# Kernel tuning notes

Hardware: AMD Instinct MI355X
Metric: run time of the kernel (lower is better)

Reference implementation:

```python
import jax, jax.numpy as jnp
import numpy as np

TEMPERATURE = 8.0  # sqrt(d_k), d_k = 64
MINIMUM_VALUE = -1e9  # stand-in for C.MINIMUM_VALUE


def setup_inputs() -> dict:
    key = jax.random.key(0)
    kq, kk, kv, km = jax.random.split(key, 4)
    B, N, D = 32, 2048, 64
    q = jax.random.normal(kq, (B, N, D), dtype=jnp.float32)
    k = jax.random.normal(kk, (B, N, D), dtype=jnp.float32)
    v = jax.random.normal(kv, (B, N, D), dtype=jnp.float32)
    mask = jax.random.randint(km, (B, N, N), 0, 2, dtype=jnp.int32)
    return {"q": q, "k": k, "v": v, "mask": mask}


def reference(q, k, v, mask):
    # scores: [B, Nq, Nk]
    attn = jnp.einsum("bqd,bkd->bqk", q, k) / TEMPERATURE
    attn = jnp.where(mask > 0, attn, MINIMUM_VALUE)
    attn = jax.nn.softmax(attn, axis=-1)
    # dropout is identity in eval / deterministic reference
    output = jnp.einsum("bqk,bkd->bqd", attn, v)
    return (output, attn)
```

## Files before the change

kernel.cpp:

```cpp
#include <hip/hip_runtime.h>

#define NB 32
#define NN 2048
#define ND 64
#define ROWS 16
#define NBLK (NB * NN / ROWS)

#define LDS_PART 65536
#define LDS_AUX  66048
#define LDS_TOTAL 70144

typedef _Float16 half8 __attribute__((ext_vector_type(8)));
typedef float f32x4 __attribute__((ext_vector_type(4)));
typedef int i32x4 __attribute__((ext_vector_type(4)));

union H4 { uint2 u; _Float16 h[4]; };

__device__ __forceinline__ f32x4 mfma16(half8 a, half8 b, f32x4 c) {
    return __builtin_amdgcn_mfma_f32_16x16x32_f16(a, b, c, 0, 0, 0);
}
#define SB() __builtin_amdgcn_sched_barrier(0)
#define LBAR() { asm volatile("s_waitcnt lgkmcnt(0)" ::: "memory"); \
                 __builtin_amdgcn_s_barrier(); \
                 __builtin_amdgcn_sched_barrier(0); }

__global__ __launch_bounds__(256) void cvt_f32_f16_k(const float* __restrict__ src,
                                                     _Float16* __restrict__ dst) {
    int i = blockIdx.x * 256 + threadIdx.x;
    const f32x4* s = (const f32x4*)src;
    f32x4 a = s[2 * i], b = s[2 * i + 1];
    half8 h;
    h[0] = (_Float16)a[0]; h[1] = (_Float16)a[1]; h[2] = (_Float16)a[2]; h[3] = (_Float16)a[3];
    h[4] = (_Float16)b[0]; h[5] = (_Float16)b[1]; h[6] = (_Float16)b[2]; h[7] = (_Float16)b[3];
    ((half8*)dst)[i] = h;
}

__global__ __launch_bounds__(256) void transpose_v_k(const float* __restrict__ v,
                                                     _Float16* __restrict__ vt) {
    __shared__ float tile[64][65];
    int b = blockIdx.x >> 5;
    int k0 = (blockIdx.x & 31) * 64;
    int t = threadIdx.x;
    {
        int dc = t & 15, kr = t >> 4;
        const f32x4* vp = (const f32x4*)(v + ((size_t)(b * NN + k0) * ND));
        #pragma unroll
        for (int i = 0; i < 4; ++i) {
            int kk = kr + i * 16;
            f32x4 x = vp[kk * 16 + dc];
            tile[kk][dc * 4 + 0] = x[0]; tile[kk][dc * 4 + 1] = x[1];
            tile[kk][dc * 4 + 2] = x[2]; tile[kk][dc * 4 + 3] = x[3];
        }
    }
    __syncthreads();
    {
        int d = t >> 2, ks = (t & 3) * 16;
        union { _Float16 hh[16]; uint4 u4[2]; } pk;
        #pragma unroll
        for (int j = 0; j < 16; ++j) pk.hh[j] = (_Float16)tile[ks + j][d];
        uint4* op = (uint4*)(vt + ((size_t)(b * ND + d) * NN + k0 + ks));
        op[0] = pk.u4[0]; op[1] = pk.u4[1];
    }
}

__global__ __launch_bounds__(256) void mask_pack_k(const int* __restrict__ mask,
                                                   unsigned long long* __restrict__ pm) {
    size_t gid = (size_t)blockIdx.x * 256 + threadIdx.x;
    size_t row = gid >> 5;
    int w = ((int)gid >> 2) & 7, lg = (int)gid & 3;
    const i32x4* mp = (const i32x4*)(mask + row * NN + w * 16 + lg * 4);
    unsigned long long bits = 0ull;
    #pragma unroll
    for (int i = 0; i < 16; i += 4) {
        i32x4 m0 = __builtin_nontemporal_load(mp + (size_t)(i + 0) * 32);
        i32x4 m1 = __builtin_nontemporal_load(mp + (size_t)(i + 1) * 32);
        i32x4 m2 = __builtin_nontemporal_load(mp + (size_t)(i + 2) * 32);
        i32x4 m3 = __builtin_nontemporal_load(mp + (size_t)(i + 3) * 32);
        unsigned b0 = (m0[0] > 0 ? 1u : 0u) | (m0[1] > 0 ? 2u : 0u) | (m0[2] > 0 ? 4u : 0u) | (m0[3] > 0 ? 8u : 0u);
        unsigned b1 = (m1[0] > 0 ? 1u : 0u) | (m1[1] > 0 ? 2u : 0u) | (m1[2] > 0 ? 4u : 0u) | (m1[3] > 0 ? 8u : 0u);
        unsigned b2 = (m2[0] > 0 ? 1u : 0u) | (m2[1] > 0 ? 2u : 0u) | (m2[2] > 0 ? 4u : 0u) | (m2[3] > 0 ? 8u : 0u);
        unsigned b3 = (m3[0] > 0 ? 1u : 0u) | (m3[1] > 0 ? 2u : 0u) | (m3[2] > 0 ? 4u : 0u) | (m3[3] > 0 ? 8u : 0u);
        bits |= (unsigned long long)(b0 | (b1 << 4) | (b2 << 8) | (b3 << 12)) << (i * 4);
    }
    pm[gid] = bits;
}

#define LDK(S, base) { \
    const _Float16* kk_ = kp + (size_t)(base) * (128 * ND); \
    S##0a = *(const half8*)(kk_);                S##0b = *(const half8*)(kk_ + 32); \
    S##1a = *(const half8*)(kk_ + 128 * ND);     S##1b = *(const half8*)(kk_ + 128 * ND + 32); \
    S##2a = *(const half8*)(kk_ + 2 * 128 * ND); S##2b = *(const half8*)(kk_ + 2 * 128 * ND + 32); \
    S##3a = *(const half8*)(kk_ + 3 * 128 * ND); S##3b = *(const half8*)(kk_ + 3 * 128 * ND + 32); }

#define CMP1(i, ka_, kb_) { \
    f32x4 acc = {0.f, 0.f, 0.f, 0.f}; \
    acc = mfma16(ka_, qf0, acc); \
    acc = mfma16(kb_, qf1, acc); \
    unsigned mb = (unsigned)(pmask >> ((i) * 4)) & 15u; \
    float e0 = (mb & 1u) ? __expf(acc[0] * 0.125f) : 0.f; \
    float e1 = (mb & 2u) ? __expf(acc[1] * 0.125f) : 0.f; \
    float e2 = (mb & 4u) ? __expf(acc[2] * 0.125f) : 0.f; \
    float e3 = (mb & 8u) ? __expf(acc[3] * 0.125f) : 0.f; \
    rsum += (e0 + e1) + (e2 + e3); \
    H4 y_; y_.h[0] = (_Float16)e0; y_.h[1] = (_Float16)e1; \
    y_.h[2] = (_Float16)e2; y_.h[3] = (_Float16)e3; \
    *(uint2*)(srow + ((((w * 16 + (i) * 128) + lg * 4) * 2) ^ sw)) = y_.u; }

#define CMP4(S, c) { CMP1((c)*4 + 0, S##0a, S##0b) CMP1((c)*4 + 1, S##1a, S##1b) \
                     CMP1((c)*4 + 2, S##2a, S##2b) CMP1((c)*4 + 3, S##3a, S##3b) }

#define LDV(S, base) { \
    const _Float16* vv_ = vp + (size_t)(kseg * 32 + (base)) * 32; \
    S##0 = *(const half8*)(vv_);       S##1 = *(const half8*)(vv_ + 32); \
    S##2 = *(const half8*)(vv_ + 64);  S##3 = *(const half8*)(vv_ + 96); \
    S##4 = *(const half8*)(vv_ + 128); S##5 = *(const half8*)(vv_ + 160); \
    S##6 = *(const half8*)(vv_ + 192); S##7 = *(const half8*)(vv_ + 224); }

#define PV1(ks_, vb_) { \
    half8 pa_ = *(const half8*)(pbase + ((((ks_) * 64) + lg * 16) ^ sw)); \
    o = mfma16(pa_, vb_, o); }

#define PV8(S, base) { PV1(kseg*32 + (base) + 0, S##0) PV1(kseg*32 + (base) + 1, S##1) \
                       PV1(kseg*32 + (base) + 2, S##2) PV1(kseg*32 + (base) + 3, S##3) \
                       PV1(kseg*32 + (base) + 4, S##4) PV1(kseg*32 + (base) + 5, S##5) \
                       PV1(kseg*32 + (base) + 6, S##6) PV1(kseg*32 + (base) + 7, S##7) }

#define NRM(jj) { \
    int colb_ = g * 8 + (jj) * 256; \
    H4 x_; x_.u = *(const uint2*)(s2 + (colb_ ^ sw2)); \
    f32x4 av_; \
    av_[0] = (float)x_.h[0] * linv; av_[1] = (float)x_.h[1] * linv; \
    av_[2] = (float)x_.h[2] * linv; av_[3] = (float)x_.h[3] * linv; \
    __builtin_nontemporal_store(av_, (f32x4*)(arow + (colb_ >> 1))); }

__global__ __launch_bounds__(512, 4) void attn_main_k(
        const _Float16* __restrict__ qh, const _Float16* __restrict__ kh,
        const _Float16* __restrict__ vtp, const unsigned long long* __restrict__ pm,
        float* __restrict__ outp, float* __restrict__ attnp) {
    extern __shared__ char smem[];

    int bid = blockIdx.x;
    int lin = (bid & 7) * (NBLK / 8) + (bid >> 3);
    int b  = lin >> 7;
    int q0 = (lin & 127) * ROWS;

    int t = threadIdx.x;
    int w = t >> 6, l = t & 63;
    int l15 = l & 15, lg = l >> 4;
    int sw = (l15 & 7) << 4;

    const _Float16* qb = qh + ((size_t)(b * NN + q0 + l15) * ND) + lg * 8;
    half8 qf0 = *(const half8*)(qb);
    half8 qf1 = *(const half8*)(qb + 32);

    unsigned long long pmask = pm[((size_t)(b * NN + q0 + l15) * 8 + w) * 4 + lg];

    const _Float16* kp = kh + (size_t)b * NN * ND + (size_t)(w * 16 + l15) * ND + lg * 8;
    char* srow = smem + l15 * 4096;
    float* part = (float*)(smem + LDS_PART);

    half8 A0a, A0b, A1a, A1b, A2a, A2b, A3a, A3b;
    half8 B0a, B0b, B1a, B1b, B2a, B2b, B3a, B3b;
    float rsum = 0.f;
    LDK(A, 0)  SB();
    LDK(B, 4)  SB();
    CMP4(A, 0) SB();
    LDK(A, 8)  SB();
    CMP4(B, 1) SB();
    LDK(B, 12) SB();
    CMP4(A, 2) SB();
    CMP4(B, 3)

    rsum += __shfl_xor(rsum, 16);
    rsum += __shfl_xor(rsum, 32);
    if (l < 16) part[w * 16 + l] = rsum;
    LBAR();

    {
        int ct = w & 3, kseg = w >> 2;
        const _Float16* vp = vtp + (size_t)(b * ND + ct * 16 + l15) * NN + lg * 8;
        char* pbase = smem + l15 * 4096;
        f32x4 o = {0.f, 0.f, 0.f, 0.f};
        half8 V0, V1, V2, V3, V4, V5, V6, V7;
        half8 W0, W1, W2, W3, W4, W5, W6, W7;
        LDV(V, 0)   SB();
        LDV(W, 8)   SB();
        PV8(V, 0)   SB();
        LDV(V, 16)  SB();
        PV8(W, 8)   SB();
        LDV(W, 24)  SB();
        PV8(V, 16)  SB();
        PV8(W, 24)

        if (kseg) *(f32x4*)(smem + LDS_AUX + ((size_t)((w - 4) * 64 + l)) * 16) = o;
        LBAR();
        if (!kseg) {
            f32x4 o2 = *(const f32x4*)(smem + LDS_AUX + ((size_t)(w * 64 + l)) * 16);
            o += o2;
            float* ob = outp + ((size_t)(b * NN + q0 + lg * 4)) * ND + ct * 16 + l15;
            #pragma unroll
            for (int rr = 0; rr < 4; ++rr) {
                int qr = lg * 4 + rr;
                float s8 = 0.f;
                #pragma unroll
                for (int pw = 0; pw < 8; ++pw) s8 += part[pw * 16 + qr];
                __builtin_nontemporal_store(o[rr] / (s8 + 1e-37f), ob + (size_t)rr * ND);
            }
        }
    }

    {
        int r = t >> 5, g = t & 31;
        float su = 0.f;
        #pragma unroll
        for (int pw = 0; pw < 8; ++pw) su += part[pw * 16 + r];
        float linv = 1.0f / (su + 1e-37f);
        char* s2 = smem + r * 4096;
        int sw2 = (r & 7) << 4;
        float* arow = attnp + ((size_t)(b * NN + q0 + r)) * NN;
        NRM(0)  NRM(1)  NRM(2)  NRM(3)
        NRM(4)  NRM(5)  NRM(6)  NRM(7)
        NRM(8)  NRM(9)  NRM(10) NRM(11)
        NRM(12) NRM(13) NRM(14) NRM(15)
    }
}

extern "C" void kernel_launch(void* const* d_in, const int* in_sizes, int n_in,
                              void* d_out, int out_size, void* d_ws, size_t ws_size,
                              hipStream_t stream) {
    const float* q = (const float*)d_in[0];
    const float* k = (const float*)d_in[1];
    const float* v = (const float*)d_in[2];
    const int* mask = (const int*)d_in[3];
    float* outp  = (float*)d_out;
    float* attnp = outp + (size_t)NB * NN * ND;

    _Float16* qh = (_Float16*)d_ws;
    _Float16* kh = qh + (size_t)NB * NN * ND;
    _Float16* vth = kh + (size_t)NB * NN * ND;
    unsigned long long* pm = (unsigned long long*)(vth + (size_t)NB * NN * ND);

    cvt_f32_f16_k<<<2048, 256, 0, stream>>>(q, qh);
    cvt_f32_f16_k<<<2048, 256, 0, stream>>>(k, kh);
    transpose_v_k<<<1024, 256, 0, stream>>>(v, vth);
    mask_pack_k<<<8192, 256, 0, stream>>>(mask, pm);
    attn_main_k<<<NBLK, 512, LDS_TOTAL, stream>>>(qh, kh, vth, pm, outp, attnp);
}
```

Measured before the change: 376.8 us.

## Fuse mask packing into attention kernel, loading int mask directly

Removes the separate mask_pack kernel and has the main attention kernel read the int32 mask directly with nontemporal loads, interleaved with the K-fragment loads in a software-pipelined schedule. This avoids writing and re-reading the packed bitmask and drops one kernel launch. In exchange the main kernel now streams 512MB of mask with more registers held for mask vectors, which may reduce occupancy or lengthen the QK phase.

Result: slower. 397.9 us (+5.6%).

```diff
diff --git a/kernel.cpp b/kernel.cpp
--- a/kernel.cpp
+++ b/kernel.cpp
@@ -63,51 +63,31 @@
     }
 }
 
-__global__ __launch_bounds__(256) void mask_pack_k(const int* __restrict__ mask,
-                                                   unsigned long long* __restrict__ pm) {
-    size_t gid = (size_t)blockIdx.x * 256 + threadIdx.x;
-    size_t row = gid >> 5;
-    int w = ((int)gid >> 2) & 7, lg = (int)gid & 3;
-    const i32x4* mp = (const i32x4*)(mask + row * NN + w * 16 + lg * 4);
-    unsigned long long bits = 0ull;
-    #pragma unroll
-    for (int i = 0; i < 16; i += 4) {
-        i32x4 m0 = __builtin_nontemporal_load(mp + (size_t)(i + 0) * 32);
-        i32x4 m1 = __builtin_nontemporal_load(mp + (size_t)(i + 1) * 32);
-        i32x4 m2 = __builtin_nontemporal_load(mp + (size_t)(i + 2) * 32);
-        i32x4 m3 = __builtin_nontemporal_load(mp + (size_t)(i + 3) * 32);
-        unsigned b0 = (m0[0] > 0 ? 1u : 0u) | (m0[1] > 0 ? 2u : 0u) | (m0[2] > 0 ? 4u : 0u) | (m0[3] > 0 ? 8u : 0u);
-        unsigned b1 = (m1[0] > 0 ? 1u : 0u) | (m1[1] > 0 ? 2u : 0u) | (m1[2] > 0 ? 4u : 0u) | (m1[3] > 0 ? 8u : 0u);
-        unsigned b2 = (m2[0] > 0 ? 1u : 0u) | (m2[1] > 0 ? 2u : 0u) | (m2[2] > 0 ? 4u : 0u) | (m2[3] > 0 ? 8u : 0u);
-        unsigned b3 = (m3[0] > 0 ? 1u : 0u) | (m3[1] > 0 ? 2u : 0u) | (m3[2] > 0 ? 4u : 0u) | (m3[3] > 0 ? 8u : 0u);
-        bits |= (unsigned long long)(b0 | (b1 << 4) | (b2 << 8) | (b3 << 12)) << (i * 4);
-    }
-    pm[gid] = bits;
-}
-
-#define LDK(S, base) { \
+#define LDK2(S, base) { \
     const _Float16* kk_ = kp + (size_t)(base) * (128 * ND); \
-    S##0a = *(const half8*)(kk_);                S##0b = *(const half8*)(kk_ + 32); \
-    S##1a = *(const half8*)(kk_ + 128 * ND);     S##1b = *(const half8*)(kk_ + 128 * ND + 32); \
-    S##2a = *(const half8*)(kk_ + 2 * 128 * ND); S##2b = *(const half8*)(kk_ + 2 * 128 * ND + 32); \
-    S##3a = *(const half8*)(kk_ + 3 * 128 * ND); S##3b = *(const half8*)(kk_ + 3 * 128 * ND + 32); }
-
-#define CMP1(i, ka_, kb_) { \
+    S##0a = *(const half8*)(kk_);              S##0b = *(const half8*)(kk_ + 32); \
+    S##1a = *(const half8*)(kk_ + 128 * ND);   S##1b = *(const half8*)(kk_ + 128 * ND + 32); }
+
+#define LDM(S, base) { \
+    S##0 = __builtin_nontemporal_load((const i32x4*)mp_ + (size_t)((base) + 0) * 32); \
+    S##1 = __builtin_nontemporal_load((const i32x4*)mp_ + (size_t)((base) + 1) * 32); \
+    S##2 = __builtin_nontemporal_load((const i32x4*)mp_ + (size_t)((base) + 2) * 32); \
+    S##3 = __builtin_nontemporal_load((const i32x4*)mp_ + (size_t)((base) + 3) * 32); }
+
+#define CMP1(i, ka_, kb_, mk_) { \
     f32x4 acc = {0.f, 0.f, 0.f, 0.f}; \
     acc = mfma16(ka_, qf0, acc); \
     acc = mfma16(kb_, qf1, acc); \
-    unsigned mb = (unsigned)(pmask >> ((i) * 4)) & 15u; \
-    float e0 = (mb & 1u) ? __expf(acc[0] * 0.125f) : 0.f; \
-    float e1 = (mb & 2u) ? __expf(acc[1] * 0.125f) : 0.f; \
-    float e2 = (mb & 4u) ? __expf(acc[2] * 0.125f) : 0.f; \
-    float e3 = (mb & 8u) ? __expf(acc[3] * 0.125f) : 0.f; \
+    float e0 = mk_[0] > 0 ? __expf(acc[0] * 0.125f) : 0.f; \
+    float e1 = mk_[1] > 0 ? __expf(acc[1] * 0.125f) : 0.f; \
+    float e2 = mk_[2] > 0 ? __expf(acc[2] * 0.125f) : 0.f; \
+    float e3 = mk_[3] > 0 ? __expf(acc[3] * 0.125f) : 0.f; \
     rsum += (e0 + e1) + (e2 + e3); \
     H4 y_; y_.h[0] = (_Float16)e0; y_.h[1] = (_Float16)e1; \
     y_.h[2] = (_Float16)e2; y_.h[3] = (_Float16)e3; \
     *(uint2*)(srow + ((((w * 16 + (i) * 128) + lg * 4) * 2) ^ sw)) = y_.u; }
 
-#define CMP4(S, c) { CMP1((c)*4 + 0, S##0a, S##0b) CMP1((c)*4 + 1, S##1a, S##1b) \
-                     CMP1((c)*4 + 2, S##2a, S##2b) CMP1((c)*4 + 3, S##3a, S##3b) }
+#define CMP2(S, c, Mx, My) { CMP1((c), S##0a, S##0b, Mx) CMP1((c) + 1, S##1a, S##1b, My) }
 
 #define LDV(S, base) { \
     const _Float16* vv_ = vp + (size_t)(kseg * 32 + (base)) * 32; \
@@ -135,7 +115,7 @@
 
 __global__ __launch_bounds__(512, 4) void attn_main_k(
         const _Float16* __restrict__ qh, const _Float16* __restrict__ kh,
-        const _Float16* __restrict__ vtp, const unsigned long long* __restrict__ pm,
+        const _Float16* __restrict__ vtp, const int* __restrict__ mask,
         float* __restrict__ outp, float* __restrict__ attnp) {
     extern __shared__ char smem[];
 
@@ -153,23 +133,33 @@
     half8 qf0 = *(const half8*)(qb);
     half8 qf1 = *(const half8*)(qb + 32);
 
-    unsigned long long pmask = pm[((size_t)(b * NN + q0 + l15) * 8 + w) * 4 + lg];
+    const int* mp_ = mask + ((size_t)(b * NN + q0 + l15)) * NN + w * 16 + lg * 4;
 
     const _Float16* kp = kh + (size_t)b * NN * ND + (size_t)(w * 16 + l15) * ND + lg * 8;
     char* srow = smem + l15 * 4096;
     float* part = (float*)(smem + LDS_PART);
 
-    half8 A0a, A0b, A1a, A1b, A2a, A2b, A3a, A3b;
-    half8 B0a, B0b, B1a, B1b, B2a, B2b, B3a, B3b;
+    i32x4 Ma0, Ma1, Ma2, Ma3, Mb0, Mb1, Mb2, Mb3;
+    half8 A0a, A0b, A1a, A1b, B0a, B0b, B1a, B1b;
     float rsum = 0.f;
-    LDK(A, 0)  SB();
-    LDK(B, 4)  SB();
-    CMP4(A, 0) SB();
-    LDK(A, 8)  SB();
-    CMP4(B, 1) SB();
-    LDK(B, 12) SB();
-    CMP4(A, 2) SB();
-    CMP4(B, 3)
+    LDM(Ma, 0)  SB();
+    LDM(Mb, 4)  SB();
+    LDK2(A, 0)  SB();
+    LDK2(B, 2)  SB();
+    CMP2(A, 0, Ma0, Ma1)  SB();
+    LDK2(A, 4)  SB();
+    CMP2(B, 2, Ma2, Ma3)  SB();
+    LDK2(B, 6)  SB();
+    CMP2(A, 4, Mb0, Mb1)  SB();
+    LDM(Ma, 8)  LDK2(A, 8)  SB();
+    CMP2(B, 6, Mb2, Mb3)  SB();
+    LDM(Mb, 12) LDK2(B, 10) SB();
+    CMP2(A, 8, Ma0, Ma1)  SB();
+    LDK2(A, 12) SB();
+    CMP2(B, 10, Ma2, Ma3) SB();
+    LDK2(B, 14) SB();
+    CMP2(A, 12, Mb0, Mb1) SB();
+    CMP2(B, 14, Mb2, Mb3)
 
     rsum += __shfl_xor(rsum, 16);
     rsum += __shfl_xor(rsum, 32);
@@ -238,11 +228,9 @@
     _Float16* qh = (_Float16*)d_ws;
     _Float16* kh = qh + (size_t)NB * NN * ND;
     _Float16* vth = kh + (size_t)NB * NN * ND;
-    unsigned long long* pm = (unsigned long long*)(vth + (size_t)NB * NN * ND);
 
     cvt_f32_f16_k<<<2048, 256, 0, stream>>>(q, qh);
     cvt_f32_f16_k<<<2048, 256, 0, stream>>>(k, kh);
     transpose_v_k<<<1024, 256, 0, stream>>>(v, vth);
-    mask_pack_k<<<8192, 256, 0, stream>>>(mask, pm);
-    attn_main_k<<<NBLK, 512, LDS_TOTAL, stream>>>(qh, kh, vth, pm, outp, attnp);
-}
+    attn_main_k<<<NBLK, 512, LDS_TOTAL, stream>>>(qh, kh, vth, mask, outp, attnp);
+}
```
